# Performance work log

Hardware: AMD Instinct MI355X
Metric: run time of the kernel (lower is better)

The kernel has to match this reference:

```python
import jax, jax.numpy as jnp
import numpy as np

LEAKY_SLOPE = 0.2  # self.alpha


def setup_inputs() -> dict:
    key = jax.random.key(0)
    k1, k2, k3 = jax.random.split(key, 3)
    E, F, R = 512, 256, 4
    h = jax.random.normal(k1, (E, F), dtype=jnp.float32)
    adj = jax.random.uniform(k2, (R, E, E), dtype=jnp.float32)
    lin_w = jax.random.normal(k3, (F,), dtype=jnp.float32) * (1.0 / np.sqrt(F))
    lin_b = jnp.zeros((1,), dtype=jnp.float32)
    return {"h": h, "adj": adj, "lin_w": lin_w, "lin_b": lin_b}


def reference(h, adj, lin_w, lin_b):
    # h: [E, F], adj: [R, E, E]
    adj_agg = jax.nn.softmax(jnp.sum(adj, axis=0), axis=1)          # [E, E]
    # pairwise elementwise product: a_input[i, j] = h_i * h_j
    a_input = h[:, None, :] * h[None, :, :]                          # [E, E, F]
    attention = jax.nn.leaky_relu(adj_agg[:, :, None] * a_input,
                                  negative_slope=LEAKY_SLOPE)        # [E, E, F]
    attention = jax.nn.softmax(attention, axis=0)                    # softmax over i
    # dropout p=0.0 / eval mode -> identity
    # Linear(F -> 1): scores[i, j] = attention[i, j] . w + b
    scores = jnp.einsum('ijf,f->ij', attention, lin_w) + lin_b[0]    # [E, E]
    alpha = jax.nn.softmax(jnp.sum(scores, axis=0)[None, :, None], axis=1)  # [1, E, 1]
    # h_prime[i, f] = sum_j attention[i, j, f] * h[j, f]
    h_prime = jnp.einsum('ijf,jf->if', attention, h)                 # [E, F]
    return jax.nn.elu(h_prime), alpha
```

## Files before the change

kernel.cpp:

```cpp
#include <hip/hip_runtime.h>


#define EE 512
#define FF 256
#define RRR 4
#define LOG2E 1.44269504088896340736f

__global__ __launch_bounds__(256) void kA(const float* __restrict__ adj,
                                          float* __restrict__ s,
                                          float* __restrict__ out) {
    const int i = blockIdx.x;
    const int t = threadIdx.x;
    if (i == 0) {
        out[EE * FF + t]       = 1.0f / EE;
        out[EE * FF + 256 + t] = 1.0f / EE;
    }
    const float* base = adj + (size_t)i * EE;
    float t0 = 0.f, t1 = 0.f;
#pragma unroll
    for (int r = 0; r < RRR; ++r) {
        t0 += base[(size_t)r * EE * EE + t];
        t1 += base[(size_t)r * EE * EE + t + 256];
    }
    const float e0 = __expf(t0);
    const float e1 = __expf(t1);
    __shared__ float red[256];
    red[t] = e0 + e1;
    __syncthreads();
    for (int off = 128; off > 0; off >>= 1) {
        if (t < off) red[t] += red[t + off];
        __syncthreads();
    }
    const float inv = 1.0f / red[0];
    s[(size_t)i * EE + t]       = e0 * inv;
    s[(size_t)i * EE + t + 256] = e1 * inv;
}

__global__ __launch_bounds__(1024, 4) void kB(const float* __restrict__ h,
                                              const float* __restrict__ s,
                                              float* __restrict__ g) {
    const int tid  = threadIdx.x;
    const int f    = tid & 255;
    const int team = tid >> 8;
    const int j0   = blockIdx.x * 2;
    __shared__ float sl[2 * EE];
    __shared__ float ps[8 * FF];
    sl[tid] = s[(size_t)(tid & 511) * EE + j0 + (tid >> 9)];
    __syncthreads();
    const float hj0 = h[(size_t)j0 * FF + f] * LOG2E;
    const float hj1 = h[(size_t)(j0 + 1) * FF + f] * LOG2E;
    float Z0 = 0.f, Z1 = 0.f;
    const int ib = team * 128;
#pragma unroll 4
    for (int ii = 0; ii < 128; ++ii) {
        const float hif = h[(size_t)(ib + ii) * FF + f];
        const float y0 = sl[ib + ii] * hif * hj0;
        const float y1 = sl[512 + ib + ii] * hif * hj1;
        Z0 += __builtin_amdgcn_exp2f(fmaxf(y0, 0.2f * y0));
        Z1 += __builtin_amdgcn_exp2f(fmaxf(y1, 0.2f * y1));
    }
    ps[(0 * 4 + team) * 256 + f] = Z0;
    ps[(1 * 4 + team) * 256 + f] = Z1;
    __syncthreads();
    if (tid < 512) {
        const int p = tid >> 8, f2 = tid & 255;
        const float Z = ps[p * 1024 + f2]       + ps[p * 1024 + 256 + f2]
                      + ps[p * 1024 + 512 + f2] + ps[p * 1024 + 768 + f2];
        g[(size_t)(j0 + p) * FF + f2] =
            h[(size_t)(j0 + p) * FF + f2] * __builtin_amdgcn_rcpf(Z);
    }
}

__global__ __launch_bounds__(1024, 4) void kC(const float* __restrict__ h,
                                              const float* __restrict__ s,
                                              const float* __restrict__ g,
                                              float* __restrict__ out) {
    const int tid  = threadIdx.x;
    const int f    = tid & 255;
    const int team = tid >> 8;
    const int i0   = blockIdx.x * 2;
    __shared__ float sl[2 * EE];
    __shared__ float ps[8 * FF];
    sl[tid] = s[(size_t)(i0 + (tid >> 9)) * EE + (tid & 511)];
    __syncthreads();
    const float hl0 = h[(size_t)i0 * FF + f] * LOG2E;
    const float hl1 = h[(size_t)(i0 + 1) * FF + f] * LOG2E;
    float a0 = 0.f, a1 = 0.f;
    const int jb = team * 128;
#pragma unroll 4
    for (int jj = 0; jj < 128; ++jj) {
        const int j = jb + jj;
        const float hjf = h[(size_t)j * FF + f];
        const float gj  = g[(size_t)j * FF + f];
        const float y0 = sl[j] * hl0 * hjf;
        const float y1 = sl[512 + j] * hl1 * hjf;
        a0 = fmaf(__builtin_amdgcn_exp2f(fmaxf(y0, 0.2f * y0)), gj, a0);
        a1 = fmaf(__builtin_amdgcn_exp2f(fmaxf(y1, 0.2f * y1)), gj, a1);
    }
    ps[(0 * 4 + team) * 256 + f] = a0;
    ps[(1 * 4 + team) * 256 + f] = a1;
    __syncthreads();
    if (tid < 512) {
        const int p = tid >> 8, f2 = tid & 255;
        const float a = ps[p * 1024 + f2]       + ps[p * 1024 + 256 + f2]
                      + ps[p * 1024 + 512 + f2] + ps[p * 1024 + 768 + f2];
        out[(size_t)(i0 + p) * FF + f2] = (a > 0.f) ? a : (__expf(a) - 1.0f);
    }
}

extern "C" void kernel_launch(void* const* d_in, const int* in_sizes, int n_in,
                              void* d_out, int out_size, void* d_ws, size_t ws_size,
                              hipStream_t stream) {
    const float* h   = (const float*)d_in[0];
    const float* adj = (const float*)d_in[1];

    float* s   = (float*)d_ws;
    float* g   = s + (size_t)EE * EE;
    float* out = (float*)d_out;

    kA<<<EE, 256, 0, stream>>>(adj, s, out);
    kB<<<EE / 2, 1024, 0, stream>>>(h, s, g);
    kC<<<EE / 2, 1024, 0, stream>>>(h, s, g, out);
}
```

Baseline: 43.60 us.

## Pack h and g into float2 and use packed-f32 vector math in kB/kC

New measurement: 42.35 us. 1.03x faster.

```diff
diff --git a/kernel.cpp b/kernel.cpp
--- a/kernel.cpp
+++ b/kernel.cpp
@@ -1,5 +1,7 @@
 #include <hip/hip_runtime.h>
 
+
+typedef float f2 __attribute__((ext_vector_type(2)));
 
 #define EE 512
 #define FF 256
@@ -38,73 +40,71 @@
 
 __global__ __launch_bounds__(1024, 4) void kB(const float* __restrict__ h,
                                               const float* __restrict__ s,
-                                              float* __restrict__ g) {
+                                              f2* __restrict__ hg) {
     const int tid  = threadIdx.x;
     const int f    = tid & 255;
     const int team = tid >> 8;
     const int j0   = blockIdx.x * 2;
-    __shared__ float sl[2 * EE];
-    __shared__ float ps[8 * FF];
-    sl[tid] = s[(size_t)(tid & 511) * EE + j0 + (tid >> 9)];
+    __shared__ f2 sl2[EE];
+    __shared__ f2 ps[4 * FF];
+    ((float*)sl2)[tid] = s[(size_t)(tid >> 1) * EE + j0 + (tid & 1)];
     __syncthreads();
-    const float hj0 = h[(size_t)j0 * FF + f] * LOG2E;
-    const float hj1 = h[(size_t)(j0 + 1) * FF + f] * LOG2E;
-    float Z0 = 0.f, Z1 = 0.f;
+    const f2 hj = {h[(size_t)j0 * FF + f] * LOG2E,
+                   h[(size_t)(j0 + 1) * FF + f] * LOG2E};
+    f2 Z = {0.f, 0.f};
     const int ib = team * 128;
 #pragma unroll 4
     for (int ii = 0; ii < 128; ++ii) {
         const float hif = h[(size_t)(ib + ii) * FF + f];
-        const float y0 = sl[ib + ii] * hif * hj0;
-        const float y1 = sl[512 + ib + ii] * hif * hj1;
-        Z0 += __builtin_amdgcn_exp2f(fmaxf(y0, 0.2f * y0));
-        Z1 += __builtin_amdgcn_exp2f(fmaxf(y1, 0.2f * y1));
+        const f2 y = sl2[ib + ii] * hif * hj;
+        const f2 m = __builtin_elementwise_max(y, 0.2f * y);
+        const f2 e = {__builtin_amdgcn_exp2f(m.x), __builtin_amdgcn_exp2f(m.y)};
+        Z += e;
     }
-    ps[(0 * 4 + team) * 256 + f] = Z0;
-    ps[(1 * 4 + team) * 256 + f] = Z1;
+    ps[team * 256 + f] = Z;
     __syncthreads();
-    if (tid < 512) {
-        const int p = tid >> 8, f2 = tid & 255;
-        const float Z = ps[p * 1024 + f2]       + ps[p * 1024 + 256 + f2]
-                      + ps[p * 1024 + 512 + f2] + ps[p * 1024 + 768 + f2];
-        g[(size_t)(j0 + p) * FF + f2] =
-            h[(size_t)(j0 + p) * FF + f2] * __builtin_amdgcn_rcpf(Z);
+    if (tid < 256) {
+        const f2 Zt = ps[f] + ps[256 + f] + ps[512 + f] + ps[768 + f];
+        const float h0 = h[(size_t)j0 * FF + f];
+        const float h1 = h[(size_t)(j0 + 1) * FF + f];
+        hg[(size_t)j0 * FF + f]       = (f2){h0, h0 * __builtin_amdgcn_rcpf(Zt.x)};
+        hg[(size_t)(j0 + 1) * FF + f] = (f2){h1, h1 * __builtin_amdgcn_rcpf(Zt.y)};
     }
 }
 
 __global__ __launch_bounds__(1024, 4) void kC(const float* __restrict__ h,
                                               const float* __restrict__ s,
-                                              const float* __restrict__ g,
+                                              const f2* __restrict__ hg,
                                               float* __restrict__ out) {
     const int tid  = threadIdx.x;
     const int f    = tid & 255;
     const int team = tid >> 8;
     const int i0   = blockIdx.x * 2;
-    __shared__ float sl[2 * EE];
-    __shared__ float ps[8 * FF];
-    sl[tid] = s[(size_t)(i0 + (tid >> 9)) * EE + (tid & 511)];
+    __shared__ f2 sl2[EE];
+    __shared__ f2 ps[4 * FF];
+    {
+        const int p = tid >> 9, j = tid & 511;
+        ((float*)sl2)[j * 2 + p] = s[(size_t)(i0 + p) * EE + j];
+    }
     __syncthreads();
-    const float hl0 = h[(size_t)i0 * FF + f] * LOG2E;
-    const float hl1 = h[(size_t)(i0 + 1) * FF + f] * LOG2E;
-    float a0 = 0.f, a1 = 0.f;
+    const f2 hl = {h[(size_t)i0 * FF + f] * LOG2E,
+                   h[(size_t)(i0 + 1) * FF + f] * LOG2E};
+    f2 acc = {0.f, 0.f};
     const int jb = team * 128;
 #pragma unroll 4
     for (int jj = 0; jj < 128; ++jj) {
-        const int j = jb + jj;
-        const float hjf = h[(size_t)j * FF + f];
-        const float gj  = g[(size_t)j * FF + f];
-        const float y0 = sl[j] * hl0 * hjf;
-        const float y1 = sl[512 + j] * hl1 * hjf;
-        a0 = fmaf(__builtin_amdgcn_exp2f(fmaxf(y0, 0.2f * y0)), gj, a0);
-        a1 = fmaf(__builtin_amdgcn_exp2f(fmaxf(y1, 0.2f * y1)), gj, a1);
+        const f2 hgv = hg[(size_t)(jb + jj) * FF + f];
+        const f2 y = sl2[jb + jj] * hgv.x * hl;
+        const f2 m = __builtin_elementwise_max(y, 0.2f * y);
+        const f2 e = {__builtin_amdgcn_exp2f(m.x), __builtin_amdgcn_exp2f(m.y)};
+        acc += e * hgv.y;
     }
-    ps[(0 * 4 + team) * 256 + f] = a0;
-    ps[(1 * 4 + team) * 256 + f] = a1;
+    ps[team * 256 + f] = acc;
     __syncthreads();
-    if (tid < 512) {
-        const int p = tid >> 8, f2 = tid & 255;
-        const float a = ps[p * 1024 + f2]       + ps[p * 1024 + 256 + f2]
-                      + ps[p * 1024 + 512 + f2] + ps[p * 1024 + 768 + f2];
-        out[(size_t)(i0 + p) * FF + f2] = (a > 0.f) ? a : (__expf(a) - 1.0f);
+    if (tid < 256) {
+        const f2 a = ps[f] + ps[256 + f] + ps[512 + f] + ps[768 + f];
+        out[(size_t)i0 * FF + f]       = (a.x > 0.f) ? a.x : (__expf(a.x) - 1.0f);
+        out[(size_t)(i0 + 1) * FF + f] = (a.y > 0.f) ? a.y : (__expf(a.y) - 1.0f);
     }
 }
 
@@ -115,10 +115,10 @@
     const float* adj = (const float*)d_in[1];
 
     float* s   = (float*)d_ws;
-    float* g   = s + (size_t)EE * EE;
+    f2*    hg  = (f2*)(s + (size_t)EE * EE);
     float* out = (float*)d_out;
 
     kA<<<EE, 256, 0, stream>>>(adj, s, out);
-    kB<<<EE / 2, 1024, 0, stream>>>(h, s, g);
-    kC<<<EE / 2, 1024, 0, stream>>>(h, s, g, out);
+    kB<<<EE / 2, 1024, 0, stream>>>(h, s, hg);
+    kC<<<EE / 2, 1024, 0, stream>>>(h, s, hg, out);
 }
```
